# Optimization experiments

Measured on AMD Instinct MI355X. Metric: run time of the kernel, lower is better.

The kernel has to match this reference:

```python
import jax, jax.numpy as jnp
import numpy as np

B, T, N, F = 32, 4096, 11, 16
NUM_LABS = 20
H = 2 * F  # refine hidden dim
LN_EPS = 1e-5


def setup_inputs() -> dict:
    key = jax.random.key(0)
    ks = jax.random.split(key, 8)
    x = jax.random.normal(ks[0], (B, T, N, F), dtype=jnp.float32)
    lab_idx = jax.random.randint(ks[1], (B,), 0, NUM_LABS)
    # projection: identity + small noise, per lab
    projection = (jnp.eye(N, dtype=jnp.float32)[None].repeat(NUM_LABS, axis=0)
                  + 0.01 * jax.random.normal(ks[2], (NUM_LABS, N, N), dtype=jnp.float32))
    bias = jnp.zeros((NUM_LABS, 1, N, F), dtype=jnp.float32)
    w1 = jax.random.normal(ks[3], (F, H), dtype=jnp.float32) / np.sqrt(F)
    b1 = jnp.zeros((H,), dtype=jnp.float32)
    ln_g = jnp.ones((H,), dtype=jnp.float32)
    ln_b = jnp.zeros((H,), dtype=jnp.float32)
    w2 = jax.random.normal(ks[4], (H, F), dtype=jnp.float32) / np.sqrt(H)
    b2 = jnp.zeros((F,), dtype=jnp.float32)
    return {"x": x, "lab_idx": lab_idx, "projection": projection, "bias": bias,
            "w1": w1, "b1": b1, "ln_g": ln_g, "ln_b": ln_b, "w2": w2, "b2": b2}


def reference(x, lab_idx, projection, bias, w1, b1, ln_g, ln_b, w2, b2):
    # gather per-sample projection / bias by lab index
    W = projection[lab_idx]          # [b, n, n]
    Bb = bias[lab_idx]               # [b, 1, n, f]
    # torch: bmm(x^T, W) then transpose -> out[b,t,m,f] = sum_n x[b,t,n,f] * W[b,n,m]
    out = jnp.einsum('btnf,bnm->btmf', x, W) + Bb
    # refine MLP: Linear -> LayerNorm -> GELU(exact) -> Linear
    h = out @ w1 + b1                                    # [b,t,n,2f]
    mu = jnp.mean(h, axis=-1, keepdims=True)
    var = jnp.var(h, axis=-1, keepdims=True)
    h = (h - mu) / jnp.sqrt(var + LN_EPS) * ln_g + ln_b
    h = jax.nn.gelu(h, approximate=False)
    return h @ w2 + b2
```

## Files before the change

### kernel.cpp

```cpp
#include <hip/hip_runtime.h>
#include <hip/hip_bf16.h>
#include <math.h>

#define BB 32
#define TT 4096
#define NN 11
#define FF 16
#define HH 32
#define LN_EPS 1e-5f

#define TOKENS_PER_BLOCK 64
#define NBLOCKS (BB * TT / TOKENS_PER_BLOCK)
#define BLOCKS_PER_BATCH (TT / TOKENS_PER_BLOCK)
#define ROW_STRIDE_B 32

typedef __attribute__((ext_vector_type(8))) short short8;
typedef __attribute__((ext_vector_type(4))) float f32x4;

union Frag { unsigned u[4]; uint4 u4; short8 v; };

__device__ __forceinline__ unsigned pack2_bf16(float a, float b) {
    __hip_bfloat162 p = __float22bfloat162_rn(make_float2(a, b));
    union { __hip_bfloat162 h; unsigned u; } cvt; cvt.h = p; return cvt.u;
}

__device__ __forceinline__ float fast_gelu(float v) {
    const float v2 = v * v;
    const float c  = fmaf(0.044715f, v2, 1.0f);
    const float t  = v * c * 1.5957691216057308f;
    const float e  = __expf(-t);
    return v * __builtin_amdgcn_rcpf(1.0f + e);
}

__global__ __launch_bounds__(256) void fused_v11b(
    const float* __restrict__ x,
    const int*   __restrict__ lab_idx,
    const float* __restrict__ proj,
    const float* __restrict__ bias,
    const float* __restrict__ w1,
    const float* __restrict__ b1,
    const float* __restrict__ ln_g,
    const float* __restrict__ ln_b,
    const float* __restrict__ w2,
    const float* __restrict__ b2,
    float*       __restrict__ out)
{
    __shared__ __align__(16) unsigned char o_st[704 * ROW_STRIDE_B];

    const int tid  = threadIdx.x;
    const int wv   = tid >> 6;
    const int lane = tid & 63;
    const int q    = lane >> 4;
    const int c    = lane & 15;
    const int tl   = tid >> 2;
    const int f4   = tid & 3;

    const int token = blockIdx.x * TOKENS_PER_BLOCK + tl;
    const int lab   = lab_idx[blockIdx.x / BLOCKS_PER_BATCH];

    const float4* xb = reinterpret_cast<const float4*>(x)    + (size_t)token * (NN * FF / 4) + f4;
    const float4* bb = reinterpret_cast<const float4*>(bias) + (size_t)lab   * (NN * FF / 4) + f4;
    const float*  Wl = proj + (size_t)lab * (NN * NN);

    float4 xv[NN];
    #pragma unroll
    for (int n = 0; n < NN; ++n) xv[n] = xb[4 * n];

    unsigned char* orow = &o_st[(tl * NN) * ROW_STRIDE_B + f4 * 8];
    #pragma unroll
    for (int m = 0; m < NN; ++m) {
        const float4 bv = bb[4 * m];
        float o0 = bv.x, o1 = bv.y, o2 = bv.z, o3 = bv.w;
        #pragma unroll
        for (int n = 0; n < NN; ++n) {
            const float wm = Wl[n * NN + m];
            o0 = fmaf(xv[n].x, wm, o0);
            o1 = fmaf(xv[n].y, wm, o1);
            o2 = fmaf(xv[n].z, wm, o2);
            o3 = fmaf(xv[n].w, wm, o3);
        }
        uint2 p;
        p.x = pack2_bf16(o0, o1);
        p.y = pack2_bf16(o2, o3);
        *reinterpret_cast<uint2*>(orow + m * ROW_STRIDE_B) = p;
    }

    Frag a1c0, a1c1, a2f;
    #pragma unroll
    for (int d = 0; d < 4; ++d) {
        const int k0 = 8 * q + 2 * d;
        float wa0 = 0.f, wa1 = 0.f, wb0 = 0.f, wb1 = 0.f;
        if (q < 2) {
            wa0 = w1[k0 * HH + c];       wa1 = w1[(k0 + 1) * HH + c];
            wb0 = w1[k0 * HH + 16 + c];  wb1 = w1[(k0 + 1) * HH + 16 + c];
        }
        a1c0.u[d] = pack2_bf16(wa0, wa1);
        a1c1.u[d] = pack2_bf16(wb0, wb1);
        a2f.u[d]  = pack2_bf16(w2[k0 * FF + c], w2[(k0 + 1) * FF + c]);
    }

    float4 b1v0 = *reinterpret_cast<const float4*>(b1 + 4 * q);
    float4 b1v1 = *reinterpret_cast<const float4*>(b1 + 16 + 4 * q);
    float4 b2v  = *reinterpret_cast<const float4*>(b2 + 4 * q);
    float4 g0   = *reinterpret_cast<const float4*>(ln_g + 4 * q);
    float4 g1   = *reinterpret_cast<const float4*>(ln_g + 16 + 4 * q);
    float4 e0   = *reinterpret_cast<const float4*>(ln_b + 4 * q);
    float4 e1   = *reinterpret_cast<const float4*>(ln_b + 16 + 4 * q);
    float g0a[4] = {g0.x, g0.y, g0.z, g0.w}, g1a[4] = {g1.x, g1.y, g1.z, g1.w};
    float e0a[4] = {e0.x, e0.y, e0.z, e0.w}, e1a[4] = {e1.x, e1.y, e1.z, e1.w};
    float b1a0[4] = {b1v0.x, b1v0.y, b1v0.z, b1v0.w};
    float b1a1[4] = {b1v1.x, b1v1.y, b1v1.z, b1v1.w};
    float b2a[4]  = {b2v.x, b2v.y, b2v.z, b2v.w};

    const size_t outrow0 = (size_t)blockIdx.x * (TOKENS_PER_BLOCK * NN) + wv * 176;
    const int srcA = (q & 1) * 32 + c;
    const int srcB = srcA + 16;

    #pragma unroll
    for (int t = 0; t < NN; ++t) {
        Frag B1;
        B1.u4 = *reinterpret_cast<const uint4*>(
            &o_st[(176 * wv + 16 * t + c) * ROW_STRIDE_B + (q & 1) * 16]);

        f32x4 accA = { b1a0[0], b1a0[1], b1a0[2], b1a0[3] };
        f32x4 accB = { b1a1[0], b1a1[1], b1a1[2], b1a1[3] };
        accA = __builtin_amdgcn_mfma_f32_16x16x32_bf16(a1c0.v, B1.v, accA, 0, 0, 0);
        accB = __builtin_amdgcn_mfma_f32_16x16x32_bf16(a1c1.v, B1.v, accB, 0, 0, 0);

        float s = 0.f, ss = 0.f;
        #pragma unroll
        for (int i = 0; i < 4; ++i) {
            s += accA[i] + accB[i];
            ss = fmaf(accA[i], accA[i], ss);
            ss = fmaf(accB[i], accB[i], ss);
        }
        s  += __shfl_xor(s, 16, 64);  s  += __shfl_xor(s, 32, 64);
        ss += __shfl_xor(ss, 16, 64); ss += __shfl_xor(ss, 32, 64);
        const float mu   = s * (1.f / HH);
        const float var  = ss * (1.f / HH) - mu * mu;
        const float rstd = rsqrtf(var + LN_EPS);
        const float nb   = -mu * rstd;

        float ga[4], gb[4];
        #pragma unroll
        for (int i = 0; i < 4; ++i) {
            ga[i] = fast_gelu(fmaf(fmaf(accA[i], rstd, nb), g0a[i], e0a[i]));
            gb[i] = fast_gelu(fmaf(fmaf(accB[i], rstd, nb), g1a[i], e1a[i]));
        }
        const unsigned c0d0 = pack2_bf16(ga[0], ga[1]);
        const unsigned c0d1 = pack2_bf16(ga[2], ga[3]);
        const unsigned c1d0 = pack2_bf16(gb[0], gb[1]);
        const unsigned c1d1 = pack2_bf16(gb[2], gb[3]);

        Frag B2;
        {
            unsigned lo, hi;
            lo = __shfl((int)c0d0, srcA, 64); hi = __shfl((int)c1d0, srcA, 64);
            B2.u[0] = (q < 2) ? lo : hi;
            lo = __shfl((int)c0d1, srcA, 64); hi = __shfl((int)c1d1, srcA, 64);
            B2.u[1] = (q < 2) ? lo : hi;
            lo = __shfl((int)c0d0, srcB, 64); hi = __shfl((int)c1d0, srcB, 64);
            B2.u[2] = (q < 2) ? lo : hi;
            lo = __shfl((int)c0d1, srcB, 64); hi = __shfl((int)c1d1, srcB, 64);
            B2.u[3] = (q < 2) ? lo : hi;
        }

        f32x4 acc2 = { b2a[0], b2a[1], b2a[2], b2a[3] };
        acc2 = __builtin_amdgcn_mfma_f32_16x16x32_bf16(a2f.v, B2.v, acc2, 0, 0, 0);

        f32x4* dst = reinterpret_cast<f32x4*>(out + (outrow0 + 16 * t + c) * FF + 4 * q);
        __builtin_nontemporal_store(acc2, dst);
    }
}

extern "C" void kernel_launch(void* const* d_in, const int* in_sizes, int n_in,
                              void* d_out, int out_size, void* d_ws, size_t ws_size,
                              hipStream_t stream) {
    const float* x       = (const float*)d_in[0];
    const int*   lab_idx = (const int*)  d_in[1];
    const float* proj    = (const float*)d_in[2];
    const float* bias    = (const float*)d_in[3];
    const float* w1      = (const float*)d_in[4];
    const float* b1      = (const float*)d_in[5];
    const float* ln_g    = (const float*)d_in[6];
    const float* ln_b    = (const float*)d_in[7];
    const float* w2      = (const float*)d_in[8];
    const float* b2      = (const float*)d_in[9];
    float* out = (float*)d_out;

    fused_v11b<<<NBLOCKS, 256, 0, stream>>>(
        x, lab_idx, proj, bias, w1, b1, ln_g, ln_b, w2, b2, out);
}
```

Baseline: 190.7 us.

## Process two token chunks per block and prefetch the second chunk's input

Each block now handles two 64-token chunks. It loads the second chunk's x into registers before running the first chunk's MLP, so global loads overlap with MFMA and GELU work. The grid is halved and launch bounds request 4 blocks per SM. Holding the extra register array raises register pressure, and the smaller grid may reduce latency hiding from parallelism.

Measured after the change: 214.0 us. 12.2% more time.

```diff
diff --git a/kernel.cpp b/kernel.cpp
--- a/kernel.cpp
+++ b/kernel.cpp
@@ -9,9 +9,9 @@
 #define HH 32
 #define LN_EPS 1e-5f
 
-#define TOKENS_PER_BLOCK 64
-#define NBLOCKS (BB * TT / TOKENS_PER_BLOCK)
-#define BLOCKS_PER_BATCH (TT / TOKENS_PER_BLOCK)
+#define TOKENS_PER_CHUNK 64
+#define NBLOCKS (BB * TT / TOKENS_PER_CHUNK / 2)
+#define CHUNKS_PER_BATCH (TT / TOKENS_PER_CHUNK)
 #define ROW_STRIDE_B 32
 
 typedef __attribute__((ext_vector_type(8))) short short8;
@@ -32,7 +32,7 @@
     return v * __builtin_amdgcn_rcpf(1.0f + e);
 }
 
-__global__ __launch_bounds__(256) void fused_v11b(
+__global__ __launch_bounds__(256, 4) void fused_v12(
     const float* __restrict__ x,
     const int*   __restrict__ lab_idx,
     const float* __restrict__ proj,
@@ -55,35 +55,17 @@
     const int tl   = tid >> 2;
     const int f4   = tid & 3;
 
-    const int token = blockIdx.x * TOKENS_PER_BLOCK + tl;
-    const int lab   = lab_idx[blockIdx.x / BLOCKS_PER_BATCH];
-
-    const float4* xb = reinterpret_cast<const float4*>(x)    + (size_t)token * (NN * FF / 4) + f4;
-    const float4* bb = reinterpret_cast<const float4*>(bias) + (size_t)lab   * (NN * FF / 4) + f4;
-    const float*  Wl = proj + (size_t)lab * (NN * NN);
-
-    float4 xv[NN];
+    const int chunk0 = blockIdx.x * 2;
+    const int lab    = lab_idx[chunk0 / CHUNKS_PER_BATCH];
+
+    const float4* xb0 = reinterpret_cast<const float4*>(x)
+                        + (size_t)(chunk0 * TOKENS_PER_CHUNK + tl) * (NN * FF / 4) + f4;
+    const float4* bb  = reinterpret_cast<const float4*>(bias) + (size_t)lab * (NN * FF / 4) + f4;
+    const float*  Wl  = proj + (size_t)lab * (NN * NN);
+
+    float4 xv0[NN];
     #pragma unroll
-    for (int n = 0; n < NN; ++n) xv[n] = xb[4 * n];
-
-    unsigned char* orow = &o_st[(tl * NN) * ROW_STRIDE_B + f4 * 8];
-    #pragma unroll
-    for (int m = 0; m < NN; ++m) {
-        const float4 bv = bb[4 * m];
-        float o0 = bv.x, o1 = bv.y, o2 = bv.z, o3 = bv.w;
-        #pragma unroll
-        for (int n = 0; n < NN; ++n) {
-            const float wm = Wl[n * NN + m];
-            o0 = fmaf(xv[n].x, wm, o0);
-            o1 = fmaf(xv[n].y, wm, o1);
-            o2 = fmaf(xv[n].z, wm, o2);
-            o3 = fmaf(xv[n].w, wm, o3);
-        }
-        uint2 p;
-        p.x = pack2_bf16(o0, o1);
-        p.y = pack2_bf16(o2, o3);
-        *reinterpret_cast<uint2*>(orow + m * ROW_STRIDE_B) = p;
-    }
+    for (int n = 0; n < NN; ++n) xv0[n] = xb0[4 * n];
 
     Frag a1c0, a1c1, a2f;
     #pragma unroll
@@ -112,65 +94,99 @@
     float b1a1[4] = {b1v1.x, b1v1.y, b1v1.z, b1v1.w};
     float b2a[4]  = {b2v.x, b2v.y, b2v.z, b2v.w};
 
-    const size_t outrow0 = (size_t)blockIdx.x * (TOKENS_PER_BLOCK * NN) + wv * 176;
     const int srcA = (q & 1) * 32 + c;
     const int srcB = srcA + 16;
 
+    auto project = [&](const float4 (&xv)[NN]) {
+        unsigned char* orow = &o_st[(tl * NN) * ROW_STRIDE_B + f4 * 8];
+        #pragma unroll
+        for (int m = 0; m < NN; ++m) {
+            const float4 bv = bb[4 * m];
+            float o0 = bv.x, o1 = bv.y, o2 = bv.z, o3 = bv.w;
+            #pragma unroll
+            for (int n = 0; n < NN; ++n) {
+                const float wm = Wl[n * NN + m];
+                o0 = fmaf(xv[n].x, wm, o0);
+                o1 = fmaf(xv[n].y, wm, o1);
+                o2 = fmaf(xv[n].z, wm, o2);
+                o3 = fmaf(xv[n].w, wm, o3);
+            }
+            uint2 p;
+            p.x = pack2_bf16(o0, o1);
+            p.y = pack2_bf16(o2, o3);
+            *reinterpret_cast<uint2*>(orow + m * ROW_STRIDE_B) = p;
+        }
+    };
+
+    auto mlp_out = [&](int chunk) {
+        const size_t outrow0 = (size_t)chunk * (TOKENS_PER_CHUNK * NN) + wv * 176;
+        #pragma unroll
+        for (int t = 0; t < NN; ++t) {
+            Frag B1;
+            B1.u4 = *reinterpret_cast<const uint4*>(
+                &o_st[(176 * wv + 16 * t + c) * ROW_STRIDE_B + (q & 1) * 16]);
+
+            f32x4 accA = { b1a0[0], b1a0[1], b1a0[2], b1a0[3] };
+            f32x4 accB = { b1a1[0], b1a1[1], b1a1[2], b1a1[3] };
+            accA = __builtin_amdgcn_mfma_f32_16x16x32_bf16(a1c0.v, B1.v, accA, 0, 0, 0);
+            accB = __builtin_amdgcn_mfma_f32_16x16x32_bf16(a1c1.v, B1.v, accB, 0, 0, 0);
+
+            float s = 0.f, ss = 0.f;
+            #pragma unroll
+            for (int i = 0; i < 4; ++i) {
+                s += accA[i] + accB[i];
+                ss = fmaf(accA[i], accA[i], ss);
+                ss = fmaf(accB[i], accB[i], ss);
+            }
+            s  += __shfl_xor(s, 16, 64);  s  += __shfl_xor(s, 32, 64);
+            ss += __shfl_xor(ss, 16, 64); ss += __shfl_xor(ss, 32, 64);
+            const float mu   = s * (1.f / HH);
+            const float var  = ss * (1.f / HH) - mu * mu;
+            const float rstd = rsqrtf(var + LN_EPS);
+            const float nb   = -mu * rstd;
+
+            float ga[4], gb[4];
+            #pragma unroll
+            for (int i = 0; i < 4; ++i) {
+                ga[i] = fast_gelu(fmaf(fmaf(accA[i], rstd, nb), g0a[i], e0a[i]));
+                gb[i] = fast_gelu(fmaf(fmaf(accB[i], rstd, nb), g1a[i], e1a[i]));
+            }
+            const unsigned c0d0 = pack2_bf16(ga[0], ga[1]);
+            const unsigned c0d1 = pack2_bf16(ga[2], ga[3]);
+            const unsigned c1d0 = pack2_bf16(gb[0], gb[1]);
+            const unsigned c1d1 = pack2_bf16(gb[2], gb[3]);
+
+            Frag B2;
+            {
+                unsigned lo, hi;
+                lo = __shfl((int)c0d0, srcA, 64); hi = __shfl((int)c1d0, srcA, 64);
+                B2.u[0] = (q < 2) ? lo : hi;
+                lo = __shfl((int)c0d1, srcA, 64); hi = __shfl((int)c1d1, srcA, 64);
+                B2.u[1] = (q < 2) ? lo : hi;
+                lo = __shfl((int)c0d0, srcB, 64); hi = __shfl((int)c1d0, srcB, 64);
+                B2.u[2] = (q < 2) ? lo : hi;
+                lo = __shfl((int)c0d1, srcB, 64); hi = __shfl((int)c1d1, srcB, 64);
+                B2.u[3] = (q < 2) ? lo : hi;
+            }
+
+            f32x4 acc2 = { b2a[0], b2a[1], b2a[2], b2a[3] };
+            acc2 = __builtin_amdgcn_mfma_f32_16x16x32_bf16(a2f.v, B2.v, acc2, 0, 0, 0);
+
+            f32x4* dst = reinterpret_cast<f32x4*>(out + (outrow0 + 16 * t + c) * FF + 4 * q);
+            __builtin_nontemporal_store(acc2, dst);
+        }
+    };
+
+    project(xv0);
+
+    float4 xv1[NN];
+    const float4* xb1 = xb0 + TOKENS_PER_CHUNK * (NN * FF / 4);
     #pragma unroll
-    for (int t = 0; t < NN; ++t) {
-        Frag B1;
-        B1.u4 = *reinterpret_cast<const uint4*>(
-            &o_st[(176 * wv + 16 * t + c) * ROW_STRIDE_B + (q & 1) * 16]);
-
-        f32x4 accA = { b1a0[0], b1a0[1], b1a0[2], b1a0[3] };
-        f32x4 accB = { b1a1[0], b1a1[1], b1a1[2], b1a1[3] };
-        accA = __builtin_amdgcn_mfma_f32_16x16x32_bf16(a1c0.v, B1.v, accA, 0, 0, 0);
-        accB = __builtin_amdgcn_mfma_f32_16x16x32_bf16(a1c1.v, B1.v, accB, 0, 0, 0);
-
-        float s = 0.f, ss = 0.f;
-        #pragma unroll
-        for (int i = 0; i < 4; ++i) {
-            s += accA[i] + accB[i];
-            ss = fmaf(accA[i], accA[i], ss);
-            ss = fmaf(accB[i], accB[i], ss);
-        }
-        s  += __shfl_xor(s, 16, 64);  s  += __shfl_xor(s, 32, 64);
-        ss += __shfl_xor(ss, 16, 64); ss += __shfl_xor(ss, 32, 64);
-        const float mu   = s * (1.f / HH);
-        const float var  = ss * (1.f / HH) - mu * mu;
-        const float rstd = rsqrtf(var + LN_EPS);
-        const float nb   = -mu * rstd;
-
-        float ga[4], gb[4];
-        #pragma unroll
-        for (int i = 0; i < 4; ++i) {
-            ga[i] = fast_gelu(fmaf(fmaf(accA[i], rstd, nb), g0a[i], e0a[i]));
-            gb[i] = fast_gelu(fmaf(fmaf(accB[i], rstd, nb), g1a[i], e1a[i]));
-        }
-        const unsigned c0d0 = pack2_bf16(ga[0], ga[1]);
-        const unsigned c0d1 = pack2_bf16(ga[2], ga[3]);
-        const unsigned c1d0 = pack2_bf16(gb[0], gb[1]);
-        const unsigned c1d1 = pack2_bf16(gb[2], gb[3]);
-
-        Frag B2;
-        {
-            unsigned lo, hi;
-            lo = __shfl((int)c0d0, srcA, 64); hi = __shfl((int)c1d0, srcA, 64);
-            B2.u[0] = (q < 2) ? lo : hi;
-            lo = __shfl((int)c0d1, srcA, 64); hi = __shfl((int)c1d1, srcA, 64);
-            B2.u[1] = (q < 2) ? lo : hi;
-            lo = __shfl((int)c0d0, srcB, 64); hi = __shfl((int)c1d0, srcB, 64);
-            B2.u[2] = (q < 2) ? lo : hi;
-            lo = __shfl((int)c0d1, srcB, 64); hi = __shfl((int)c1d1, srcB, 64);
-            B2.u[3] = (q < 2) ? lo : hi;
-        }
-
-        f32x4 acc2 = { b2a[0], b2a[1], b2a[2], b2a[3] };
-        acc2 = __builtin_amdgcn_mfma_f32_16x16x32_bf16(a2f.v, B2.v, acc2, 0, 0, 0);
-
-        f32x4* dst = reinterpret_cast<f32x4*>(out + (outrow0 + 16 * t + c) * FF + 4 * q);
-        __builtin_nontemporal_store(acc2, dst);
-    }
+    for (int n = 0; n < NN; ++n) xv1[n] = xb1[4 * n];
+
+    mlp_out(chunk0);
+    project(xv1);
+    mlp_out(chunk0 + 1);
 }
 
 extern "C" void kernel_launch(void* const* d_in, const int* in_sizes, int n_in,
@@ -188,6 +204,6 @@
     const float* b2      = (const float*)d_in[9];
     float* out = (float*)d_out;
 
-    fused_v11b<<<NBLOCKS, 256, 0, stream>>>(
+    fused_v12<<<NBLOCKS, 256, 0, stream>>>(
         x, lab_idx, proj, bias, w1, b1, ln_g, ln_b, w2, b2, out);
 }
```

## Process two token chunks per block, prefetching second chunk during first MLP

Applied to the files above, without the earlier changes.

Each block now handles two consecutive 64-token chunks, loading the second chunk's inputs into registers before running the first chunk's MLP so global loads overlap compute. The grid is halved, launch bounds request 4 blocks per CU, and output stores become regular instead of nontemporal. It trades extra register pressure and fewer blocks for better latency hiding.

Result: slower. 199.9 us (+4.8%).

```diff
diff --git a/kernel.cpp b/kernel.cpp
--- a/kernel.cpp
+++ b/kernel.cpp
@@ -9,9 +9,9 @@
 #define HH 32
 #define LN_EPS 1e-5f
 
-#define TOKENS_PER_BLOCK 64
-#define NBLOCKS (BB * TT / TOKENS_PER_BLOCK)
-#define BLOCKS_PER_BATCH (TT / TOKENS_PER_BLOCK)
+#define TOKENS_PER_CHUNK 64
+#define NBLOCKS (BB * TT / TOKENS_PER_CHUNK / 2)
+#define CHUNKS_PER_BATCH (TT / TOKENS_PER_CHUNK)
 #define ROW_STRIDE_B 32
 
 typedef __attribute__((ext_vector_type(8))) short short8;
@@ -32,7 +32,83 @@
     return v * __builtin_amdgcn_rcpf(1.0f + e);
 }
 
-__global__ __launch_bounds__(256) void fused_v11b(
+#define PROJ_BODY(XV)                                                            \
+    do {                                                                         \
+        unsigned char* orow = &o_st[(tl * NN) * ROW_STRIDE_B + f4 * 8];          \
+        _Pragma("unroll")                                                        \
+        for (int m = 0; m < NN; ++m) {                                           \
+            const float4 bv = bb[4 * m];                                         \
+            float o0 = bv.x, o1 = bv.y, o2 = bv.z, o3 = bv.w;                    \
+            _Pragma("unroll")                                                    \
+            for (int n = 0; n < NN; ++n) {                                       \
+                const float wm = Wl[n * NN + m];                                 \
+                o0 = fmaf(XV[n].x, wm, o0);                                      \
+                o1 = fmaf(XV[n].y, wm, o1);                                      \
+                o2 = fmaf(XV[n].z, wm, o2);                                      \
+                o3 = fmaf(XV[n].w, wm, o3);                                      \
+            }                                                                    \
+            uint2 p;                                                             \
+            p.x = pack2_bf16(o0, o1);                                            \
+            p.y = pack2_bf16(o2, o3);                                            \
+            *reinterpret_cast<uint2*>(orow + m * ROW_STRIDE_B) = p;              \
+        }                                                                        \
+    } while (0)
+
+#define TLOOP_BODY(CH)                                                           \
+    do {                                                                         \
+        const size_t outrow0 = (size_t)(CH) * (TOKENS_PER_CHUNK * NN) + wv * 176;\
+        _Pragma("unroll")                                                        \
+        for (int t = 0; t < NN; ++t) {                                           \
+            Frag B1;                                                             \
+            B1.u4 = *reinterpret_cast<const uint4*>(                             \
+                &o_st[(176 * wv + 16 * t + c) * ROW_STRIDE_B + (q & 1) * 16]);   \
+            f32x4 accA = { b1a0[0], b1a0[1], b1a0[2], b1a0[3] };                 \
+            f32x4 accB = { b1a1[0], b1a1[1], b1a1[2], b1a1[3] };                 \
+            accA = __builtin_amdgcn_mfma_f32_16x16x32_bf16(a1c0.v, B1.v, accA, 0, 0, 0); \
+            accB = __builtin_amdgcn_mfma_f32_16x16x32_bf16(a1c1.v, B1.v, accB, 0, 0, 0); \
+            float s = 0.f, ss = 0.f;                                             \
+            _Pragma("unroll")                                                    \
+            for (int i = 0; i < 4; ++i) {                                        \
+                s += accA[i] + accB[i];                                          \
+                ss = fmaf(accA[i], accA[i], ss);                                 \
+                ss = fmaf(accB[i], accB[i], ss);                                 \
+            }                                                                    \
+            s  += __shfl_xor(s, 16, 64);  s  += __shfl_xor(s, 32, 64);           \
+            ss += __shfl_xor(ss, 16, 64); ss += __shfl_xor(ss, 32, 64);          \
+            const float mu   = s * (1.f / HH);                                   \
+            const float var  = ss * (1.f / HH) - mu * mu;                        \
+            const float rstd = rsqrtf(var + LN_EPS);                             \
+            const float nb   = -mu * rstd;                                       \
+            float ga[4], gb[4];                                                  \
+            _Pragma("unroll")                                                    \
+            for (int i = 0; i < 4; ++i) {                                        \
+                ga[i] = fast_gelu(fmaf(fmaf(accA[i], rstd, nb), g0a[i], e0a[i]));\
+                gb[i] = fast_gelu(fmaf(fmaf(accB[i], rstd, nb), g1a[i], e1a[i]));\
+            }                                                                    \
+            const unsigned c0d0 = pack2_bf16(ga[0], ga[1]);                      \
+            const unsigned c0d1 = pack2_bf16(ga[2], ga[3]);                      \
+            const unsigned c1d0 = pack2_bf16(gb[0], gb[1]);                      \
+            const unsigned c1d1 = pack2_bf16(gb[2], gb[3]);                      \
+            Frag B2;                                                             \
+            {                                                                    \
+                unsigned lo, hi;                                                 \
+                lo = __shfl((int)c0d0, srcA, 64); hi = __shfl((int)c1d0, srcA, 64); \
+                B2.u[0] = (q < 2) ? lo : hi;                                     \
+                lo = __shfl((int)c0d1, srcA, 64); hi = __shfl((int)c1d1, srcA, 64); \
+                B2.u[1] = (q < 2) ? lo : hi;                                     \
+                lo = __shfl((int)c0d0, srcB, 64); hi = __shfl((int)c1d0, srcB, 64); \
+                B2.u[2] = (q < 2) ? lo : hi;                                     \
+                lo = __shfl((int)c0d1, srcB, 64); hi = __shfl((int)c1d1, srcB, 64); \
+                B2.u[3] = (q < 2) ? lo : hi;                                     \
+            }                                                                    \
+            f32x4 acc2 = { b2a[0], b2a[1], b2a[2], b2a[3] };                     \
+            acc2 = __builtin_amdgcn_mfma_f32_16x16x32_bf16(a2f.v, B2.v, acc2, 0, 0, 0); \
+            float4* dst = reinterpret_cast<float4*>(out + (outrow0 + 16 * t + c) * FF + 4 * q); \
+            *dst = make_float4(acc2[0], acc2[1], acc2[2], acc2[3]);              \
+        }                                                                        \
+    } while (0)
+
+__global__ __launch_bounds__(256, 4) void fused_v14(
     const float* __restrict__ x,
     const int*   __restrict__ lab_idx,
     const float* __restrict__ proj,
@@ -55,34 +131,25 @@
     const int tl   = tid >> 2;
     const int f4   = tid & 3;
 
-    const int token = blockIdx.x * TOKENS_PER_BLOCK + tl;
-    const int lab   = lab_idx[blockIdx.x / BLOCKS_PER_BATCH];
-
-    const float4* xb = reinterpret_cast<const float4*>(x)    + (size_t)token * (NN * FF / 4) + f4;
-    const float4* bb = reinterpret_cast<const float4*>(bias) + (size_t)lab   * (NN * FF / 4) + f4;
+    const int chunk0 = blockIdx.x * 2;
+    const int lab    = lab_idx[chunk0 / CHUNKS_PER_BATCH];
+
+    const float4* xb = reinterpret_cast<const float4*>(x)
+                       + (size_t)(chunk0 * TOKENS_PER_CHUNK + tl) * (NN * FF / 4) + f4;
+    const float4* bb = reinterpret_cast<const float4*>(bias) + (size_t)lab * (NN * FF / 4) + f4;
     const float*  Wl = proj + (size_t)lab * (NN * NN);
 
-    float4 xv[NN];
+    float4 xvA[NN];
     #pragma unroll
-    for (int n = 0; n < NN; ++n) xv[n] = xb[4 * n];
-
-    unsigned char* orow = &o_st[(tl * NN) * ROW_STRIDE_B + f4 * 8];
-    #pragma unroll
-    for (int m = 0; m < NN; ++m) {
-        const float4 bv = bb[4 * m];
-        float o0 = bv.x, o1 = bv.y, o2 = bv.z, o3 = bv.w;
+    for (int n = 0; n < NN; ++n) xvA[n] = xb[4 * n];
+
+    PROJ_BODY(xvA);
+
+    float4 xvB[NN];
+    {
+        const float4* xb1 = xb + TOKENS_PER_CHUNK * (NN * FF / 4);
         #pragma unroll
-        for (int n = 0; n < NN; ++n) {
-            const float wm = Wl[n * NN + m];
-            o0 = fmaf(xv[n].x, wm, o0);
-            o1 = fmaf(xv[n].y, wm, o1);
-            o2 = fmaf(xv[n].z, wm, o2);
-            o3 = fmaf(xv[n].w, wm, o3);
-        }
-        uint2 p;
-        p.x = pack2_bf16(o0, o1);
-        p.y = pack2_bf16(o2, o3);
-        *reinterpret_cast<uint2*>(orow + m * ROW_STRIDE_B) = p;
+        for (int n = 0; n < NN; ++n) xvB[n] = xb1[4 * n];
     }
 
     Frag a1c0, a1c1, a2f;
@@ -112,65 +179,12 @@
     float b1a1[4] = {b1v1.x, b1v1.y, b1v1.z, b1v1.w};
     float b2a[4]  = {b2v.x, b2v.y, b2v.z, b2v.w};
 
-    const size_t outrow0 = (size_t)blockIdx.x * (TOKENS_PER_BLOCK * NN) + wv * 176;
     const int srcA = (q & 1) * 32 + c;
     const int srcB = srcA + 16;
 
-    #pragma unroll
-    for (int t = 0; t < NN; ++t) {
-        Frag B1;
-        B1.u4 = *reinterpret_cast<const uint4*>(
-            &o_st[(176 * wv + 16 * t + c) * ROW_STRIDE_B + (q & 1) * 16]);
-
-        f32x4 accA = { b1a0[0], b1a0[1], b1a0[2], b1a0[3] };
-        f32x4 accB = { b1a1[0], b1a1[1], b1a1[2], b1a1[3] };
-        accA = __builtin_amdgcn_mfma_f32_16x16x32_bf16(a1c0.v, B1.v, accA, 0, 0, 0);
-        accB = __builtin_amdgcn_mfma_f32_16x16x32_bf16(a1c1.v, B1.v, accB, 0, 0, 0);
-
-        float s = 0.f, ss = 0.f;
-        #pragma unroll
-        for (int i = 0; i < 4; ++i) {
-            s += accA[i] + accB[i];
-            ss = fmaf(accA[i], accA[i], ss);
-            ss = fmaf(accB[i], accB[i], ss);
-        }
-        s  += __shfl_xor(s, 16, 64);  s  += __shfl_xor(s, 32, 64);
-        ss += __shfl_xor(ss, 16, 64); ss += __shfl_xor(ss, 32, 64);
-        const float mu   = s * (1.f / HH);
-        const float var  = ss * (1.f / HH) - mu * mu;
-        const float rstd = rsqrtf(var + LN_EPS);
-        const float nb   = -mu * rstd;
-
-        float ga[4], gb[4];
-        #pragma unroll
-        for (int i = 0; i < 4; ++i) {
-            ga[i] = fast_gelu(fmaf(fmaf(accA[i], rstd, nb), g0a[i], e0a[i]));
-            gb[i] = fast_gelu(fmaf(fmaf(accB[i], rstd, nb), g1a[i], e1a[i]));
-        }
-        const unsigned c0d0 = pack2_bf16(ga[0], ga[1]);
-        const unsigned c0d1 = pack2_bf16(ga[2], ga[3]);
-        const unsigned c1d0 = pack2_bf16(gb[0], gb[1]);
-        const unsigned c1d1 = pack2_bf16(gb[2], gb[3]);
-
-        Frag B2;
-        {
-            unsigned lo, hi;
-            lo = __shfl((int)c0d0, srcA, 64); hi = __shfl((int)c1d0, srcA, 64);
-            B2.u[0] = (q < 2) ? lo : hi;
-            lo = __shfl((int)c0d1, srcA, 64); hi = __shfl((int)c1d1, srcA, 64);
-            B2.u[1] = (q < 2) ? lo : hi;
-            lo = __shfl((int)c0d0, srcB, 64); hi = __shfl((int)c1d0, srcB, 64);
-            B2.u[2] = (q < 2) ? lo : hi;
-            lo = __shfl((int)c0d1, srcB, 64); hi = __shfl((int)c1d1, srcB, 64);
-            B2.u[3] = (q < 2) ? lo : hi;
-        }
-
-        f32x4 acc2 = { b2a[0], b2a[1], b2a[2], b2a[3] };
-        acc2 = __builtin_amdgcn_mfma_f32_16x16x32_bf16(a2f.v, B2.v, acc2, 0, 0, 0);
-
-        f32x4* dst = reinterpret_cast<f32x4*>(out + (outrow0 + 16 * t + c) * FF + 4 * q);
-        __builtin_nontemporal_store(acc2, dst);
-    }
+    TLOOP_BODY(chunk0);
+    PROJ_BODY(xvB);
+    TLOOP_BODY(chunk0 + 1);
 }
 
 extern "C" void kernel_launch(void* const* d_in, const int* in_sizes, int n_in,
@@ -188,6 +202,6 @@
     const float* b2      = (const float*)d_in[9];
     float* out = (float*)d_out;
 
-    fused_v11b<<<NBLOCKS, 256, 0, stream>>>(
+    fused_v14<<<NBLOCKS, 256, 0, stream>>>(
         x, lab_idx, proj, bias, w1, b1, ln_g, ln_b, w2, b2, out);
 }
```
